# Kernel optimization log

Hardware: AMD Instinct MI355X
Metric: run time of the kernel (lower is better)

Reference implementation:

```python
import jax, jax.numpy as jnp
import numpy as np

DEPTH, HEADS, K, EPS = 4, 8, 3, 1e-5
DIM, CIN, COUT = 128, 64, 64


def conv1x1(x, w, b=None):
    y = jnp.einsum('oi,bihw->bohw', w, x)
    return y if b is None else y + b[None, :, None, None]


def dilated_conv3x3(x, w, b, d):
    y = jax.lax.conv_general_dilated(
        x, w, window_strides=(1, 1), padding=[(d, d), (d, d)],
        rhs_dilation=(d, d), dimension_numbers=('NCHW', 'OIHW', 'NCHW'))
    return y + b[None, :, None, None]


def batchnorm_train(x, g, b):
    # BatchNorm2d in training mode: biased batch stats over (B,H,W)
    mu = jnp.mean(x, axis=(0, 2, 3), keepdims=True)
    var = jnp.var(x, axis=(0, 2, 3), keepdims=True)
    return (x - mu) * jax.lax.rsqrt(var + EPS) * g[None, :, None, None] + b[None, :, None, None]


def unfold3(x):
    # nn.Unfold(k=3, pad=1): (B,C,H,W) -> (B,C,k*k,H,W), patch index row-major (dy,dx)
    B, C, H, W = x.shape
    p = K // 2
    xp = jnp.pad(x, ((0, 0), (0, 0), (p, p), (p, p)))
    return jnp.stack([xp[:, :, dy:dy + H, dx:dx + W]
                      for dy in range(K) for dx in range(K)], axis=2)


def local_self_attention(x, qkv_w, fc_w, fc_b):
    B, C, H, W = x.shape
    c = C // HEADS
    scale = c ** -0.5
    qkv = conv1x1(x, qkv_w)                      # (B,3C,H,W)
    q, k, v = jnp.split(qkv, 3, axis=1)
    shape6 = lambda t: unfold3(t).reshape(B, HEADS, c, K * K, H, W)
    q, k, v = shape6(q) * scale, shape6(k), shape6(v)
    # NOTE: original einsum labels dim2 (channels/head) as n/m and dim3 (k^2) as the
    # contracted axis, i.e. channel-attention contracted over the 9 patch positions.
    dots = jnp.einsum('bhnkij,bhmkij->bhnmij', q, k)   # (B,h,c,c,H,W)
    attn = jax.nn.softmax(dots, axis=3)
    out = jnp.einsum('bhnmij,bhmkij->bhnkij', attn, v)  # (B,h,c,k^2,H,W)
    out = out.reshape(B, C, K * K, H, W).sum(axis=2)
    return conv1x1(out, fc_w, fc_b) + x


def setup_inputs() -> dict:
    key = jax.random.key(0)
    ks = jax.random.split(key, 12)
    s = 0.05
    return {
        'x': jax.random.normal(ks[0], (2, CIN, 96, 96), jnp.float32),
        'w_in': jax.random.normal(ks[1], (DIM, CIN), jnp.float32) * s,
        'b_in': jnp.zeros((DIM,), jnp.float32),
        'conv_w': jax.random.normal(ks[2], (DEPTH, DIM, DIM, 3, 3), jnp.float32) * s,
        'conv_b': jnp.zeros((DEPTH, DIM), jnp.float32),
        'bn_g': jnp.ones((DEPTH, DIM), jnp.float32),
        'bn_b': jnp.zeros((DEPTH, DIM), jnp.float32),
        'qkv_w': jax.random.normal(ks[3], (DEPTH, 3 * DIM, DIM), jnp.float32) * s,
        'fc_w': jax.random.normal(ks[4], (DEPTH, DIM, DIM), jnp.float32) * s,
        'fc_b': jnp.zeros((DEPTH, DIM), jnp.float32),
        'w_out': jax.random.normal(ks[5], (COUT, DIM), jnp.float32) * s,
        'b_out': jnp.zeros((COUT,), jnp.float32),
    }


def reference(x, w_in, b_in, conv_w, conv_b, bn_g, bn_b, qkv_w, fc_w, fc_b, w_out, b_out):
    h = conv1x1(x, w_in, b_in)
    for i in range(DEPTH):
        d = 2 ** i
        h = jax.nn.relu(batchnorm_train(dilated_conv3x3(h, conv_w[i], conv_b[i], d), bn_g[i], bn_b[i]))
        h = local_self_attention(h, qkv_w[i], fc_w[i], fc_b[i])
    return conv1x1(h, w_out, b_out)
```

## Files before the change

kernel.cpp:

```cpp
#include <hip/hip_runtime.h>
#include <math.h>

typedef __attribute__((ext_vector_type(8))) short bf16x8;
typedef __attribute__((ext_vector_type(4))) float f32x4;
typedef __attribute__((ext_vector_type(4))) unsigned short us4;
typedef __attribute__((ext_vector_type(8))) unsigned short us8;

constexpr int BB = 2;
constexpr int CC = 128;
constexpr int HH = 96, WW = 96;
constexpr int PP = HH * WW;
constexpr int NN = BB * PP;
constexpr int CONV_BLKS = NN / 48;

__device__ __forceinline__ float bf2f(unsigned short u) {
    return __uint_as_float(((unsigned)u) << 16);
}
__device__ __forceinline__ unsigned short f2bf(float f) {
    unsigned u = __float_as_uint(f);
    unsigned r = u + 0x7fff + ((u >> 16) & 1);
    return (unsigned short)(r >> 16);
}

__global__ __launch_bounds__(256)
void k_wconv(const float* __restrict__ conv_w, const float* __restrict__ qkv_w,
             const float* __restrict__ fc_w, const float* __restrict__ w_in,
             const float* __restrict__ w_out,
             unsigned short* __restrict__ wcv, unsigned short* __restrict__ wqkv,
             unsigned short* __restrict__ wfc, unsigned short* __restrict__ wi,
             unsigned short* __restrict__ wo)
{
    int gid = blockIdx.x * 256 + threadIdx.x;
    if (gid < 589824) {
        int L = gid / 147456, r = gid % 147456;
        int o = r / 1152, k = r % 1152;
        int t = k / 128, c = k % 128;
        float v = conv_w[(((size_t)(L * 128 + o) * 128 + c) * 9) + t];
        wcv[gid] = f2bf(v);
    } else if (gid < 786432) {
        int g = gid - 589824;
        int o = (g % 49152) / 128;
        float v = qkv_w[g] * (o < 128 ? 0.25f : 1.0f);
        wqkv[g] = f2bf(v);
    } else if (gid < 851968) {
        int g = gid - 786432;
        wfc[g] = f2bf(fc_w[g]);
    } else if (gid < 860160) {
        int g = gid - 851968;
        wi[g] = f2bf(w_in[g]);
    } else if (gid < 868352) {
        int g = gid - 860160;
        wo[g] = f2bf(w_out[g]);
    }
}

__global__ __launch_bounds__(256)
void k_xconv(const float* __restrict__ x, unsigned short* __restrict__ xT)
{
    int n = blockIdx.x * 256 + threadIdx.x;
    int b = n / PP, p = n - b * PP;
    unsigned short* dst = xT + (size_t)n * 64;
    #pragma unroll
    for (int cg = 0; cg < 16; ++cg) {
        us4 st;
        #pragma unroll
        for (int r = 0; r < 4; ++r)
            st[r] = f2bf(x[((size_t)(b * 64 + cg * 4 + r)) * PP + p]);
        *reinterpret_cast<us4*>(dst + cg * 4) = st;
    }
}

template<int DIL>
__global__ __launch_bounds__(384)
void k_conv(const unsigned short* __restrict__ W,
            const unsigned short* __restrict__ act,
            float* __restrict__ y,
            float* __restrict__ parts,
            const unsigned short* __restrict__ zp)
{
    int tid = threadIdx.x;
    int lane = tid & 63, wv = tid >> 6;
    int wm = wv & 1, wz = wv >> 1;
    int l15 = lane & 15, kg = lane >> 4;

    int n_base = blockIdx.x * 48;
    int o_base = wm * 64;

    const unsigned short* wbase[4];
    #pragma unroll
    for (int fm = 0; fm < 4; ++fm)
        wbase[fm] = W + (size_t)(o_base + fm * 16 + l15) * 1152 + kg * 8;

    const unsigned short* bbase[3];
    int iF[3], jF[3];
    #pragma unroll
    for (int fn = 0; fn < 3; ++fn) {
        int n = n_base + fn * 16 + l15;
        bbase[fn] = act + (size_t)n * 128 + kg * 8;
        int pix = n % PP;
        iF[fn] = pix / WW;
        jF[fn] = pix % WW;
    }

    f32x4 acc[4][3];
    #pragma unroll
    for (int fm = 0; fm < 4; ++fm)
        #pragma unroll
        for (int fn = 0; fn < 3; ++fn)
            acc[fm][fn] = (f32x4){0.f, 0.f, 0.f, 0.f};

    const unsigned short* zpk = zp + kg * 8;
    int t0 = wz * 3;
    #pragma unroll
    for (int tt = 0; tt < 3; ++tt) {
        int t = t0 + tt;
        int oy = (t / 3 - 1) * DIL, ox = (t % 3 - 1) * DIL;
        int disp = (oy * WW + ox) * 128;
        const unsigned short* baddr[3];
        #pragma unroll
        for (int fn = 0; fn < 3; ++fn) {
            bool v = ((unsigned)(iF[fn] + oy) < (unsigned)HH) &&
                     ((unsigned)(jF[fn] + ox) < (unsigned)WW);
            baddr[fn] = v ? (bbase[fn] + disp) : zpk;
        }
        #pragma unroll
        for (int c0 = 0; c0 < 128; c0 += 32) {
            bf16x8 a[4], b[3];
            #pragma unroll
            for (int fm = 0; fm < 4; ++fm)
                a[fm] = *reinterpret_cast<const bf16x8*>(wbase[fm] + t * 128 + c0);
            #pragma unroll
            for (int fn = 0; fn < 3; ++fn)
                b[fn] = *reinterpret_cast<const bf16x8*>(baddr[fn] + c0);
            #pragma unroll
            for (int fm = 0; fm < 4; ++fm)
                #pragma unroll
                for (int fn = 0; fn < 3; ++fn)
                    acc[fm][fn] = __builtin_amdgcn_mfma_f32_16x16x32_bf16(
                        a[fm], b[fn], acc[fm][fn], 0, 0, 0);
        }
    }

    __shared__ float red[4][48][64];
    if (wz) {
        int s = wm * 2 + wz - 1;
        #pragma unroll
        for (int fm = 0; fm < 4; ++fm)
            #pragma unroll
            for (int fn = 0; fn < 3; ++fn)
                #pragma unroll
                for (int r = 0; r < 4; ++r)
                    red[s][fm * 12 + fn * 4 + r][lane] = acc[fm][fn][r];
    }
    __syncthreads();
    if (wz == 0) {
        #pragma unroll
        for (int fm = 0; fm < 4; ++fm)
            #pragma unroll
            for (int fn = 0; fn < 3; ++fn)
                #pragma unroll
                for (int r = 0; r < 4; ++r)
                    acc[fm][fn][r] += red[wm * 2][fm * 12 + fn * 4 + r][lane] +
                                      red[wm * 2 + 1][fm * 12 + fn * 4 + r][lane];

        #pragma unroll
        for (int fm = 0; fm < 4; ++fm) {
            int o0 = o_base + fm * 16 + kg * 4;
            #pragma unroll
            for (int fn = 0; fn < 3; ++fn) {
                int n = n_base + fn * 16 + l15;
                *reinterpret_cast<f32x4*>(y + (size_t)n * 128 + o0) = acc[fm][fn];
            }
        }

        #pragma unroll
        for (int fm = 0; fm < 4; ++fm) {
            #pragma unroll
            for (int r = 0; r < 4; ++r) {
                float s = 0.f, s2 = 0.f;
                #pragma unroll
                for (int fn = 0; fn < 3; ++fn) {
                    float v = acc[fm][fn][r];
                    s += v; s2 += v * v;
                }
                #pragma unroll
                for (int m = 1; m <= 8; m <<= 1) {
                    s  += __shfl_xor(s,  m, 64);
                    s2 += __shfl_xor(s2, m, 64);
                }
                if (l15 == 0) {
                    int c = o_base + fm * 16 + kg * 4 + r;
                    parts[(size_t)blockIdx.x * 256 + c]       = s;
                    parts[(size_t)blockIdx.x * 256 + 128 + c] = s2;
                }
            }
        }
    }
}

template<int WM, int WN, int F, int MODE>
__global__ __launch_bounds__(WM * WN * 64)
void k_gemm(const unsigned short* __restrict__ W,
            const unsigned short* __restrict__ act,
            const float* __restrict__ bias,
            const unsigned short* __restrict__ resid,
            void* __restrict__ outp,
            int Kw, int Cin, int Cout)
{
    int tid = threadIdx.x;
    int lane = tid & 63, wv = tid >> 6;
    int wm = wv % WM, wn = wv / WM;
    int l15 = lane & 15, kg = lane >> 4;

    int n_base = blockIdx.x * (WN * 16 * F) + wn * 16 * F;
    int o_base = blockIdx.y * (WM * 64) + wm * 64;

    const unsigned short* wbase[4];
    #pragma unroll
    for (int fm = 0; fm < 4; ++fm) {
        int o = o_base + fm * 16 + l15;
        wbase[fm] = W + (size_t)o * Kw + kg * 8;
    }

    const unsigned short* bbase[F];
    #pragma unroll
    for (int fn = 0; fn < F; ++fn) {
        int n = n_base + fn * 16 + l15;
        bbase[fn] = act + (size_t)n * Cin + kg * 8;
    }

    f32x4 acc[4][F];
    #pragma unroll
    for (int fm = 0; fm < 4; ++fm)
        #pragma unroll
        for (int fn = 0; fn < F; ++fn)
            acc[fm][fn] = (f32x4){0.f, 0.f, 0.f, 0.f};

    #pragma unroll
    for (int k0 = 0; k0 < 128; k0 += 32) {
        if (k0 >= Cin) break;
        bf16x8 a[4], b[F];
        #pragma unroll
        for (int fm = 0; fm < 4; ++fm)
            a[fm] = *reinterpret_cast<const bf16x8*>(wbase[fm] + k0);
        #pragma unroll
        for (int fn = 0; fn < F; ++fn)
            b[fn] = *reinterpret_cast<const bf16x8*>(bbase[fn] + k0);
        #pragma unroll
        for (int fm = 0; fm < 4; ++fm)
            #pragma unroll
            for (int fn = 0; fn < F; ++fn)
                acc[fm][fn] = __builtin_amdgcn_mfma_f32_16x16x32_bf16(
                    a[fm], b[fn], acc[fm][fn], 0, 0, 0);
    }

    #pragma unroll
    for (int fm = 0; fm < 4; ++fm) {
        #pragma unroll
        for (int fn = 0; fn < F; ++fn) {
            f32x4 v = acc[fm][fn];
            int n = n_base + fn * 16 + l15;
            int o0 = o_base + fm * 16 + kg * 4;
            if constexpr (MODE == 0 || MODE == 2) {
                if (bias) {
                    #pragma unroll
                    for (int r = 0; r < 4; ++r) v[r] += bias[o0 + r];
                }
                if constexpr (MODE == 2) {
                    us4 rv = *reinterpret_cast<const us4*>(resid + (size_t)n * Cout + o0);
                    #pragma unroll
                    for (int r = 0; r < 4; ++r) v[r] += bf2f(rv[r]);
                }
                us4 st;
                #pragma unroll
                for (int r = 0; r < 4; ++r) st[r] = f2bf(v[r]);
                *reinterpret_cast<us4*>((unsigned short*)outp + (size_t)n * Cout + o0) = st;
            } else {
                int b_ = n / PP, p = n - b_ * PP;
                float* op = (float*)outp;
                #pragma unroll
                for (int r = 0; r < 4; ++r)
                    op[((size_t)(b_ * Cout + o0 + r)) * PP + p] = v[r] + bias[o0 + r];
            }
        }
    }
}

__global__ __launch_bounds__(384)
void k_bnfin(const float* __restrict__ partials, const float* __restrict__ g,
             const float* __restrict__ b, float* __restrict__ scsh)
{
    int c = blockIdx.x;
    int t = threadIdx.x;
    float s  = partials[(size_t)t * 256 + c];
    float s2 = partials[(size_t)t * 256 + 128 + c];
    #pragma unroll
    for (int m = 32; m > 0; m >>= 1) {
        s  += __shfl_down(s,  m, 64);
        s2 += __shfl_down(s2, m, 64);
    }
    __shared__ float ls[6], ls2[6];
    int wid = t >> 6;
    if ((t & 63) == 0) { ls[wid] = s; ls2[wid] = s2; }
    __syncthreads();
    if (t == 0) {
        float S = 0.f, S2 = 0.f;
        #pragma unroll
        for (int w = 0; w < 6; ++w) { S += ls[w]; S2 += ls2[w]; }
        const float inv = 1.f / (float)NN;
        float mu = S * inv;
        float var = S2 * inv - mu * mu;
        float sc = g[c] * rsqrtf(var + 1e-5f);
        scsh[c] = sc;
        scsh[128 + c] = b[c] - mu * sc;
    }
}

__global__ __launch_bounds__(256)
void k_bnrelu(const float* __restrict__ y, const float* __restrict__ scsh,
              unsigned short* __restrict__ h)
{
    int gid = blockIdx.x * 256 + threadIdx.x;
    int c0 = (gid * 4) & 127;
    size_t idx = (size_t)gid * 4;
    f32x4 v = *reinterpret_cast<const f32x4*>(y + idx);
    us4 st;
    #pragma unroll
    for (int r = 0; r < 4; ++r) {
        float f = fmaxf(fmaf(v[r], scsh[c0 + r], scsh[128 + c0 + r]), 0.f);
        st[r] = f2bf(f);
    }
    *reinterpret_cast<us4*>(h + idx) = st;
}

__global__ __launch_bounds__(256)
void k_attn(const unsigned short* __restrict__ qkv, unsigned short* __restrict__ att)
{
    int gid = blockIdx.x * 256 + threadIdx.x;
    int ng   = gid & 3;
    int head = (gid >> 2) & 7;
    int n    = gid >> 5;
    int pix = n % PP;
    int i = pix / WW, j = pix % WW;
    int hc = head * 16;
    const unsigned short* base = qkv + (size_t)n * 384;

    float dots[4][16];
    float vs[16];
    #pragma unroll
    for (int m = 0; m < 16; ++m) vs[m] = 0.f;
    #pragma unroll
    for (int nn = 0; nn < 4; ++nn)
        #pragma unroll
        for (int m = 0; m < 16; ++m) dots[nn][m] = 0.f;

    #pragma unroll
    for (int dy = 0; dy < 3; ++dy) {
        #pragma unroll
        for (int dx = 0; dx < 3; ++dx) {
            if (!(((unsigned)(i + dy - 1) < (unsigned)HH) &&
                  ((unsigned)(j + dx - 1) < (unsigned)WW))) continue;
            const unsigned short* pb = base + ((dy - 1) * WW + (dx - 1)) * 384;
            us4 q4 = *reinterpret_cast<const us4*>(pb + hc + ng * 4);
            us8 k0 = *reinterpret_cast<const us8*>(pb + 128 + hc);
            us8 k1 = *reinterpret_cast<const us8*>(pb + 128 + hc + 8);
            us8 v0 = *reinterpret_cast<const us8*>(pb + 256 + hc);
            us8 v1 = *reinterpret_cast<const us8*>(pb + 256 + hc + 8);
            float kf[16];
            #pragma unroll
            for (int e = 0; e < 8; ++e) {
                kf[e] = bf2f(k0[e]);
                kf[8 + e] = bf2f(k1[e]);
                vs[e] += bf2f(v0[e]);
                vs[8 + e] += bf2f(v1[e]);
            }
            #pragma unroll
            for (int nn = 0; nn < 4; ++nn) {
                float qf = bf2f(q4[nn]);
                #pragma unroll
                for (int m = 0; m < 16; ++m)
                    dots[nn][m] = fmaf(qf, kf[m], dots[nn][m]);
            }
        }
    }

    us4 st;
    #pragma unroll
    for (int nn = 0; nn < 4; ++nn) {
        float mx = dots[nn][0];
        #pragma unroll
        for (int m = 1; m < 16; ++m) mx = fmaxf(mx, dots[nn][m]);
        float den = 0.f, o = 0.f;
        #pragma unroll
        for (int m = 0; m < 16; ++m) {
            float e = __expf(dots[nn][m] - mx);
            den += e;
            o = fmaf(e, vs[m], o);
        }
        st[nn] = f2bf(o / den);
    }
    *reinterpret_cast<us4*>(att + (size_t)n * CC + hc + ng * 4) = st;
}

extern "C" void kernel_launch(void* const* d_in, const int* in_sizes, int n_in,
                              void* d_out, int out_size, void* d_ws, size_t ws_size,
                              hipStream_t stream)
{
    const float* x      = (const float*)d_in[0];
    const float* w_in   = (const float*)d_in[1];
    const float* b_in   = (const float*)d_in[2];
    const float* conv_w = (const float*)d_in[3];
    const float* bn_g   = (const float*)d_in[5];
    const float* bn_b   = (const float*)d_in[6];
    const float* qkv_w  = (const float*)d_in[7];
    const float* fc_w   = (const float*)d_in[8];
    const float* fc_b   = (const float*)d_in[9];
    const float* w_out  = (const float*)d_in[10];
    const float* b_out  = (const float*)d_in[11];

    char* ws = (char*)d_ws;
    unsigned short* zp    = (unsigned short*)(ws);
    unsigned short* wcv   = (unsigned short*)(ws + 4096);
    unsigned short* wqkv  = (unsigned short*)(ws + 1183744);
    unsigned short* wfc   = (unsigned short*)(ws + 1576960);
    unsigned short* wi    = (unsigned short*)(ws + 1708032);
    unsigned short* wo    = (unsigned short*)(ws + 1724416);
    unsigned short* xT    = (unsigned short*)(ws + 1740800);
    unsigned short* bufA  = (unsigned short*)(ws + 4100096);
    float*          ybuf  = (float*)        (ws + 8818688);
    unsigned short* hbuf  = (unsigned short*)(ws + 18255872);
    unsigned short* qkvb  = (unsigned short*)(ws + 22974464);
    unsigned short* attb  = (unsigned short*)(ws + 37130240);
    float*          parts = (float*)        (ws + 41848832);
    float*          scsh  = (float*)        (ws + 42242048);

    hipMemsetAsync(zp, 0, 4096, stream);

    k_wconv<<<3392, 256, 0, stream>>>(conv_w, qkv_w, fc_w, w_in, w_out,
                                      wcv, wqkv, wfc, wi, wo);
    k_xconv<<<NN / 256, 256, 0, stream>>>(x, xT);

    k_gemm<1, 2, 3, 0><<<dim3(192, 2), 128, 0, stream>>>(
        wi, xT, b_in, nullptr, bufA, 64, 64, 128);

    for (int L = 0; L < 4; ++L) {
        const unsigned short* wc = wcv + (size_t)L * 147456;
        switch (L) {
            case 0: k_conv<1><<<CONV_BLKS, 384, 0, stream>>>(wc, bufA, ybuf, parts, zp); break;
            case 1: k_conv<2><<<CONV_BLKS, 384, 0, stream>>>(wc, bufA, ybuf, parts, zp); break;
            case 2: k_conv<4><<<CONV_BLKS, 384, 0, stream>>>(wc, bufA, ybuf, parts, zp); break;
            case 3: k_conv<8><<<CONV_BLKS, 384, 0, stream>>>(wc, bufA, ybuf, parts, zp); break;
        }
        k_bnfin<<<128, 384, 0, stream>>>(parts, bn_g + L * 128, bn_b + L * 128, scsh);
        k_bnrelu<<<2304, 256, 0, stream>>>(ybuf, scsh, hbuf);

        k_gemm<1, 2, 3, 0><<<dim3(192, 6), 128, 0, stream>>>(
            wqkv + (size_t)L * 49152, hbuf, nullptr, nullptr, qkvb, 128, 128, 384);

        k_attn<<<2304, 256, 0, stream>>>(qkvb, attb);

        k_gemm<1, 2, 3, 2><<<dim3(192, 2), 128, 0, stream>>>(
            wfc + (size_t)L * 16384, attb, fc_b + L * 128, hbuf, bufA, 128, 128, 128);
    }

    k_gemm<1, 2, 3, 3><<<dim3(192, 1), 128, 0, stream>>>(
        wo, bufA, b_out, nullptr, (float*)d_out, 128, 128, 64);
}
```

Before: 465.4 us.

## Fuse local attention with fc projection and split conv output channels across grid

The attention kernel now writes its per-pixel outputs into a swizzled shared-memory tile and immediately runs the 128x128 fc projection with MFMA, adding bias and residual before storing. This removes the attention intermediate buffer round trip and one kernel launch per layer. Separately, the dilated conv kernel now splits the two 64-channel output halves across a second grid dimension with 192-thread blocks instead of one 384-thread block. That doubles the block count and halves shared memory per block, at the cost of reading each activation tile twice.

Result: no change. 474.4 us (+1.9%).

```diff
diff --git a/kernel.cpp b/kernel.cpp
--- a/kernel.cpp
+++ b/kernel.cpp
@@ -71,7 +71,7 @@
 }
 
 template<int DIL>
-__global__ __launch_bounds__(384)
+__global__ __launch_bounds__(192)
 void k_conv(const unsigned short* __restrict__ W,
             const unsigned short* __restrict__ act,
             float* __restrict__ y,
@@ -79,12 +79,11 @@
             const unsigned short* __restrict__ zp)
 {
     int tid = threadIdx.x;
-    int lane = tid & 63, wv = tid >> 6;
-    int wm = wv & 1, wz = wv >> 1;
+    int lane = tid & 63, wz = tid >> 6;
     int l15 = lane & 15, kg = lane >> 4;
 
     int n_base = blockIdx.x * 48;
-    int o_base = wm * 64;
+    int o_base = blockIdx.y * 64;
 
     const unsigned short* wbase[4];
     #pragma unroll
@@ -141,16 +140,15 @@
         }
     }
 
-    __shared__ float red[4][48][64];
+    __shared__ float red[2][48][64];
     if (wz) {
-        int s = wm * 2 + wz - 1;
         #pragma unroll
         for (int fm = 0; fm < 4; ++fm)
             #pragma unroll
             for (int fn = 0; fn < 3; ++fn)
                 #pragma unroll
                 for (int r = 0; r < 4; ++r)
-                    red[s][fm * 12 + fn * 4 + r][lane] = acc[fm][fn][r];
+                    red[wz - 1][fm * 12 + fn * 4 + r][lane] = acc[fm][fn][r];
     }
     __syncthreads();
     if (wz == 0) {
@@ -160,8 +158,8 @@
             for (int fn = 0; fn < 3; ++fn)
                 #pragma unroll
                 for (int r = 0; r < 4; ++r)
-                    acc[fm][fn][r] += red[wm * 2][fm * 12 + fn * 4 + r][lane] +
-                                      red[wm * 2 + 1][fm * 12 + fn * 4 + r][lane];
+                    acc[fm][fn][r] += red[0][fm * 12 + fn * 4 + r][lane] +
+                                      red[1][fm * 12 + fn * 4 + r][lane];
 
         #pragma unroll
         for (int fm = 0; fm < 4; ++fm) {
@@ -203,7 +201,6 @@
 void k_gemm(const unsigned short* __restrict__ W,
             const unsigned short* __restrict__ act,
             const float* __restrict__ bias,
-            const unsigned short* __restrict__ resid,
             void* __restrict__ outp,
             int Kw, int Cin, int Cout)
 {
@@ -261,15 +258,10 @@
             f32x4 v = acc[fm][fn];
             int n = n_base + fn * 16 + l15;
             int o0 = o_base + fm * 16 + kg * 4;
-            if constexpr (MODE == 0 || MODE == 2) {
+            if constexpr (MODE == 0) {
                 if (bias) {
                     #pragma unroll
                     for (int r = 0; r < 4; ++r) v[r] += bias[o0 + r];
-                }
-                if constexpr (MODE == 2) {
-                    us4 rv = *reinterpret_cast<const us4*>(resid + (size_t)n * Cout + o0);
-                    #pragma unroll
-                    for (int r = 0; r < 4; ++r) v[r] += bf2f(rv[r]);
                 }
                 us4 st;
                 #pragma unroll
@@ -334,72 +326,139 @@
 }
 
 __global__ __launch_bounds__(256)
-void k_attn(const unsigned short* __restrict__ qkv, unsigned short* __restrict__ att)
-{
-    int gid = blockIdx.x * 256 + threadIdx.x;
-    int ng   = gid & 3;
-    int head = (gid >> 2) & 7;
-    int n    = gid >> 5;
-    int pix = n % PP;
-    int i = pix / WW, j = pix % WW;
-    int hc = head * 16;
-    const unsigned short* base = qkv + (size_t)n * 384;
-
-    float dots[4][16];
-    float vs[16];
-    #pragma unroll
-    for (int m = 0; m < 16; ++m) vs[m] = 0.f;
-    #pragma unroll
-    for (int nn = 0; nn < 4; ++nn)
-        #pragma unroll
-        for (int m = 0; m < 16; ++m) dots[nn][m] = 0.f;
-
-    #pragma unroll
-    for (int dy = 0; dy < 3; ++dy) {
-        #pragma unroll
-        for (int dx = 0; dx < 3; ++dx) {
-            if (!(((unsigned)(i + dy - 1) < (unsigned)HH) &&
-                  ((unsigned)(j + dx - 1) < (unsigned)WW))) continue;
-            const unsigned short* pb = base + ((dy - 1) * WW + (dx - 1)) * 384;
-            us4 q4 = *reinterpret_cast<const us4*>(pb + hc + ng * 4);
-            us8 k0 = *reinterpret_cast<const us8*>(pb + 128 + hc);
-            us8 k1 = *reinterpret_cast<const us8*>(pb + 128 + hc + 8);
-            us8 v0 = *reinterpret_cast<const us8*>(pb + 256 + hc);
-            us8 v1 = *reinterpret_cast<const us8*>(pb + 256 + hc + 8);
-            float kf[16];
-            #pragma unroll
-            for (int e = 0; e < 8; ++e) {
-                kf[e] = bf2f(k0[e]);
-                kf[8 + e] = bf2f(k1[e]);
-                vs[e] += bf2f(v0[e]);
-                vs[8 + e] += bf2f(v1[e]);
+void k_attnfc(const unsigned short* __restrict__ qkv,
+              const unsigned short* __restrict__ wfc,
+              const float* __restrict__ fcb,
+              const unsigned short* __restrict__ resid,
+              unsigned short* __restrict__ out)
+{
+    __shared__ unsigned short atile[32 * 128];
+    int tid = threadIdx.x;
+    int n_base = blockIdx.x * 32;
+
+    #pragma unroll 1
+    for (int u = 0; u < 4; ++u) {
+        int unit = u * 256 + tid;
+        int pl   = unit >> 5;
+        int head = (unit >> 2) & 7;
+        int ng   = unit & 3;
+        int n    = n_base + pl;
+        int pix  = n % PP;
+        int i = pix / WW, j = pix % WW;
+        int hc = head * 16;
+        const unsigned short* base = qkv + (size_t)n * 384;
+
+        float dots[4][16];
+        float vs[16];
+        #pragma unroll
+        for (int m = 0; m < 16; ++m) vs[m] = 0.f;
+        #pragma unroll
+        for (int nn = 0; nn < 4; ++nn)
+            #pragma unroll
+            for (int m = 0; m < 16; ++m) dots[nn][m] = 0.f;
+
+        #pragma unroll
+        for (int dy = 0; dy < 3; ++dy) {
+            #pragma unroll
+            for (int dx = 0; dx < 3; ++dx) {
+                if (!(((unsigned)(i + dy - 1) < (unsigned)HH) &&
+                      ((unsigned)(j + dx - 1) < (unsigned)WW))) continue;
+                const unsigned short* pb = base + ((dy - 1) * WW + (dx - 1)) * 384;
+                us4 q4 = *reinterpret_cast<const us4*>(pb + hc + ng * 4);
+                us8 k0 = *reinterpret_cast<const us8*>(pb + 128 + hc);
+                us8 k1 = *reinterpret_cast<const us8*>(pb + 128 + hc + 8);
+                us8 v0 = *reinterpret_cast<const us8*>(pb + 256 + hc);
+                us8 v1 = *reinterpret_cast<const us8*>(pb + 256 + hc + 8);
+                float kf[16];
+                #pragma unroll
+                for (int e = 0; e < 8; ++e) {
+                    kf[e] = bf2f(k0[e]);
+                    kf[8 + e] = bf2f(k1[e]);
+                    vs[e] += bf2f(v0[e]);
+                    vs[8 + e] += bf2f(v1[e]);
+                }
+                #pragma unroll
+                for (int nn = 0; nn < 4; ++nn) {
+                    float qf = bf2f(q4[nn]);
+                    #pragma unroll
+                    for (int m = 0; m < 16; ++m)
+                        dots[nn][m] = fmaf(qf, kf[m], dots[nn][m]);
+                }
             }
-            #pragma unroll
-            for (int nn = 0; nn < 4; ++nn) {
-                float qf = bf2f(q4[nn]);
-                #pragma unroll
-                for (int m = 0; m < 16; ++m)
-                    dots[nn][m] = fmaf(qf, kf[m], dots[nn][m]);
+        }
+
+        us4 st;
+        #pragma unroll
+        for (int nn = 0; nn < 4; ++nn) {
+            float mx = dots[nn][0];
+            #pragma unroll
+            for (int m = 1; m < 16; ++m) mx = fmaxf(mx, dots[nn][m]);
+            float den = 0.f, o = 0.f;
+            #pragma unroll
+            for (int m = 0; m < 16; ++m) {
+                float e = __expf(dots[nn][m] - mx);
+                den += e;
+                o = fmaf(e, vs[m], o);
             }
-        }
-    }
-
-    us4 st;
-    #pragma unroll
-    for (int nn = 0; nn < 4; ++nn) {
-        float mx = dots[nn][0];
-        #pragma unroll
-        for (int m = 1; m < 16; ++m) mx = fmaxf(mx, dots[nn][m]);
-        float den = 0.f, o = 0.f;
-        #pragma unroll
-        for (int m = 0; m < 16; ++m) {
-            float e = __expf(dots[nn][m] - mx);
-            den += e;
-            o = fmaf(e, vs[m], o);
-        }
-        st[nn] = f2bf(o / den);
-    }
-    *reinterpret_cast<us4*>(att + (size_t)n * CC + hc + ng * 4) = st;
+            st[nn] = f2bf(o / den);
+        }
+        int off = (pl * 256 + (hc + ng * 4) * 2) ^ ((pl & 7) << 4);
+        *reinterpret_cast<us4*>(reinterpret_cast<char*>(atile) + off) = st;
+    }
+    __syncthreads();
+
+    int lane = tid & 63, wvv = tid >> 6;
+    int l15 = lane & 15, kg = lane >> 4;
+    int o_base = wvv * 32;
+
+    const unsigned short* wbase[2];
+    #pragma unroll
+    for (int fm = 0; fm < 2; ++fm)
+        wbase[fm] = wfc + (size_t)(o_base + fm * 16 + l15) * 128 + kg * 8;
+
+    f32x4 acc[2][2];
+    #pragma unroll
+    for (int fm = 0; fm < 2; ++fm)
+        #pragma unroll
+        for (int fn = 0; fn < 2; ++fn)
+            acc[fm][fn] = (f32x4){0.f, 0.f, 0.f, 0.f};
+
+    #pragma unroll
+    for (int k0 = 0; k0 < 128; k0 += 32) {
+        bf16x8 a[2], b[2];
+        #pragma unroll
+        for (int fm = 0; fm < 2; ++fm)
+            a[fm] = *reinterpret_cast<const bf16x8*>(wbase[fm] + k0);
+        #pragma unroll
+        for (int fn = 0; fn < 2; ++fn) {
+            int pl2 = fn * 16 + l15;
+            int off = (pl2 * 256 + (k0 + kg * 8) * 2) ^ ((pl2 & 7) << 4);
+            b[fn] = *reinterpret_cast<const bf16x8*>(reinterpret_cast<char*>(atile) + off);
+        }
+        #pragma unroll
+        for (int fm = 0; fm < 2; ++fm)
+            #pragma unroll
+            for (int fn = 0; fn < 2; ++fn)
+                acc[fm][fn] = __builtin_amdgcn_mfma_f32_16x16x32_bf16(
+                    a[fm], b[fn], acc[fm][fn], 0, 0, 0);
+    }
+
+    #pragma unroll
+    for (int fm = 0; fm < 2; ++fm) {
+        #pragma unroll
+        for (int fn = 0; fn < 2; ++fn) {
+            f32x4 v = acc[fm][fn];
+            int n = n_base + fn * 16 + l15;
+            int o0 = o_base + fm * 16 + kg * 4;
+            us4 rv = *reinterpret_cast<const us4*>(resid + (size_t)n * 128 + o0);
+            #pragma unroll
+            for (int r = 0; r < 4; ++r) v[r] += fcb[o0 + r] + bf2f(rv[r]);
+            us4 st;
+            #pragma unroll
+            for (int r = 0; r < 4; ++r) st[r] = f2bf(v[r]);
+            *reinterpret_cast<us4*>(out + (size_t)n * 128 + o0) = st;
+        }
+    }
 }
 
 extern "C" void kernel_launch(void* const* d_in, const int* in_sizes, int n_in,
@@ -430,7 +489,6 @@
     float*          ybuf  = (float*)        (ws + 8818688);
     unsigned short* hbuf  = (unsigned short*)(ws + 18255872);
     unsigned short* qkvb  = (unsigned short*)(ws + 22974464);
-    unsigned short* attb  = (unsigned short*)(ws + 37130240);
     float*          parts = (float*)        (ws + 41848832);
     float*          scsh  = (float*)        (ws + 42242048);
 
@@ -441,28 +499,26 @@
     k_xconv<<<NN / 256, 256, 0, stream>>>(x, xT);
 
     k_gemm<1, 2, 3, 0><<<dim3(192, 2), 128, 0, stream>>>(
-        wi, xT, b_in, nullptr, bufA, 64, 64, 128);
+        wi, xT, b_in, bufA, 64, 64, 128);
 
     for (int L = 0; L < 4; ++L) {
         const unsigned short* wc = wcv + (size_t)L * 147456;
         switch (L) {
-            case 0: k_conv<1><<<CONV_BLKS, 384, 0, stream>>>(wc, bufA, ybuf, parts, zp); break;
-            case 1: k_conv<2><<<CONV_BLKS, 384, 0, stream>>>(wc, bufA, ybuf, parts, zp); break;
-            case 2: k_conv<4><<<CONV_BLKS, 384, 0, stream>>>(wc, bufA, ybuf, parts, zp); break;
-            case 3: k_conv<8><<<CONV_BLKS, 384, 0, stream>>>(wc, bufA, ybuf, parts, zp); break;
+            case 0: k_conv<1><<<dim3(CONV_BLKS, 2), 192, 0, stream>>>(wc, bufA, ybuf, parts, zp); break;
+            case 1: k_conv<2><<<dim3(CONV_BLKS, 2), 192, 0, stream>>>(wc, bufA, ybuf, parts, zp); break;
+            case 2: k_conv<4><<<dim3(CONV_BLKS, 2), 192, 0, stream>>>(wc, bufA, ybuf, parts, zp); break;
+            case 3: k_conv<8><<<dim3(CONV_BLKS, 2), 192, 0, stream>>>(wc, bufA, ybuf, parts, zp); break;
         }
         k_bnfin<<<128, 384, 0, stream>>>(parts, bn_g + L * 128, bn_b + L * 128, scsh);
         k_bnrelu<<<2304, 256, 0, stream>>>(ybuf, scsh, hbuf);
 
         k_gemm<1, 2, 3, 0><<<dim3(192, 6), 128, 0, stream>>>(
-            wqkv + (size_t)L * 49152, hbuf, nullptr, nullptr, qkvb, 128, 128, 384);
-
-        k_attn<<<2304, 256, 0, stream>>>(qkvb, attb);
-
-        k_gemm<1, 2, 3, 2><<<dim3(192, 2), 128, 0, stream>>>(
-            wfc + (size_t)L * 16384, attb, fc_b + L * 128, hbuf, bufA, 128, 128, 128);
+            wqkv + (size_t)L * 49152, hbuf, nullptr, qkvb, 128, 128, 384);
+
+        k_attnfc<<<576, 256, 0, stream>>>(
+            qkvb, wfc + (size_t)L * 16384, fc_b + L * 128, hbuf, bufA);
     }
 
     k_gemm<1, 2, 3, 3><<<dim3(192, 1), 128, 0, stream>>>(
-        wo, bufA, b_out, nullptr, (float*)d_out, 128, 128, 64);
-}
+        wo, bufA, b_out, (float*)d_out, 128, 128, 64);
+}
```

## Stage attention rows in LDS and split conv blocks over output channels

Applied to the files above, without the earlier changes.

The local attention kernel now has each block load a three-row band of q/k/v for one head pair into shared memory. Its 3x3 neighbourhood reads then come from LDS rather than repeatedly from global memory. The dilated conv kernel moves the two output-channel halves from separate waves in one 384-thread block to a second grid dimension of 192-thread blocks, which halves the reduction scratch and doubles the block count. The roughly 60 KB LDS tile per attention block limits how many blocks fit on a CU, and each conv block now reloads its activation tile for each output half.

After: 462.2 us. About the same (-0.7%).

```diff
diff --git a/kernel.cpp b/kernel.cpp
--- a/kernel.cpp
+++ b/kernel.cpp
@@ -71,7 +71,7 @@
 }
 
 template<int DIL>
-__global__ __launch_bounds__(384)
+__global__ __launch_bounds__(192)
 void k_conv(const unsigned short* __restrict__ W,
             const unsigned short* __restrict__ act,
             float* __restrict__ y,
@@ -79,12 +79,11 @@
             const unsigned short* __restrict__ zp)
 {
     int tid = threadIdx.x;
-    int lane = tid & 63, wv = tid >> 6;
-    int wm = wv & 1, wz = wv >> 1;
+    int lane = tid & 63, wz = tid >> 6;
     int l15 = lane & 15, kg = lane >> 4;
 
     int n_base = blockIdx.x * 48;
-    int o_base = wm * 64;
+    int o_base = blockIdx.y * 64;
 
     const unsigned short* wbase[4];
     #pragma unroll
@@ -141,16 +140,15 @@
         }
     }
 
-    __shared__ float red[4][48][64];
+    __shared__ float red[2][48][64];
     if (wz) {
-        int s = wm * 2 + wz - 1;
         #pragma unroll
         for (int fm = 0; fm < 4; ++fm)
             #pragma unroll
             for (int fn = 0; fn < 3; ++fn)
                 #pragma unroll
                 for (int r = 0; r < 4; ++r)
-                    red[s][fm * 12 + fn * 4 + r][lane] = acc[fm][fn][r];
+                    red[wz - 1][fm * 12 + fn * 4 + r][lane] = acc[fm][fn][r];
     }
     __syncthreads();
     if (wz == 0) {
@@ -160,8 +158,8 @@
             for (int fn = 0; fn < 3; ++fn)
                 #pragma unroll
                 for (int r = 0; r < 4; ++r)
-                    acc[fm][fn][r] += red[wm * 2][fm * 12 + fn * 4 + r][lane] +
-                                      red[wm * 2 + 1][fm * 12 + fn * 4 + r][lane];
+                    acc[fm][fn][r] += red[0][fm * 12 + fn * 4 + r][lane] +
+                                      red[1][fm * 12 + fn * 4 + r][lane];
 
         #pragma unroll
         for (int fm = 0; fm < 4; ++fm) {
@@ -334,72 +332,98 @@
 }
 
 __global__ __launch_bounds__(256)
-void k_attn(const unsigned short* __restrict__ qkv, unsigned short* __restrict__ att)
-{
-    int gid = blockIdx.x * 256 + threadIdx.x;
-    int ng   = gid & 3;
-    int head = (gid >> 2) & 7;
-    int n    = gid >> 5;
-    int pix = n % PP;
-    int i = pix / WW, j = pix % WW;
-    int hc = head * 16;
-    const unsigned short* base = qkv + (size_t)n * 384;
-
-    float dots[4][16];
-    float vs[16];
-    #pragma unroll
-    for (int m = 0; m < 16; ++m) vs[m] = 0.f;
-    #pragma unroll
-    for (int nn = 0; nn < 4; ++nn)
-        #pragma unroll
-        for (int m = 0; m < 16; ++m) dots[nn][m] = 0.f;
-
-    #pragma unroll
-    for (int dy = 0; dy < 3; ++dy) {
-        #pragma unroll
-        for (int dx = 0; dx < 3; ++dx) {
-            if (!(((unsigned)(i + dy - 1) < (unsigned)HH) &&
-                  ((unsigned)(j + dx - 1) < (unsigned)WW))) continue;
-            const unsigned short* pb = base + ((dy - 1) * WW + (dx - 1)) * 384;
-            us4 q4 = *reinterpret_cast<const us4*>(pb + hc + ng * 4);
-            us8 k0 = *reinterpret_cast<const us8*>(pb + 128 + hc);
-            us8 k1 = *reinterpret_cast<const us8*>(pb + 128 + hc + 8);
-            us8 v0 = *reinterpret_cast<const us8*>(pb + 256 + hc);
-            us8 v1 = *reinterpret_cast<const us8*>(pb + 256 + hc + 8);
-            float kf[16];
-            #pragma unroll
-            for (int e = 0; e < 8; ++e) {
-                kf[e] = bf2f(k0[e]);
-                kf[8 + e] = bf2f(k1[e]);
-                vs[e] += bf2f(v0[e]);
-                vs[8 + e] += bf2f(v1[e]);
-            }
-            #pragma unroll
-            for (int nn = 0; nn < 4; ++nn) {
-                float qf = bf2f(q4[nn]);
-                #pragma unroll
-                for (int m = 0; m < 16; ++m)
-                    dots[nn][m] = fmaf(qf, kf[m], dots[nn][m]);
-            }
-        }
-    }
-
-    us4 st;
-    #pragma unroll
-    for (int nn = 0; nn < 4; ++nn) {
-        float mx = dots[nn][0];
-        #pragma unroll
-        for (int m = 1; m < 16; ++m) mx = fmaxf(mx, dots[nn][m]);
-        float den = 0.f, o = 0.f;
-        #pragma unroll
-        for (int m = 0; m < 16; ++m) {
-            float e = __expf(dots[nn][m] - mx);
-            den += e;
-            o = fmaf(e, vs[m], o);
-        }
-        st[nn] = f2bf(o / den);
-    }
-    *reinterpret_cast<us4*>(att + (size_t)n * CC + hc + ng * 4) = st;
+void k_attn2(const unsigned short* __restrict__ qkv, unsigned short* __restrict__ att)
+{
+    __shared__ unsigned short tile[288 * 104];
+    int tid = threadIdx.x;
+    int br = blockIdx.x;
+    int hp = blockIdx.y;
+    int b = br / HH, i = br - (br / HH) * HH;
+
+    #pragma unroll 1
+    for (int it = 0; it < 14; ++it) {
+        int idx = it * 256 + tid;
+        if (idx < 3456) {
+            int pp = idx / 12;
+            int rem = idx - pp * 12;
+            int s = rem >> 2, u8 = rem & 3;
+            int rr = pp / 96, col = pp - rr * 96;
+            int ai = i + rr - 1;
+            us8 val = {0, 0, 0, 0, 0, 0, 0, 0};
+            if ((unsigned)ai < (unsigned)HH) {
+                int n = b * PP + ai * WW + col;
+                val = *reinterpret_cast<const us8*>(
+                    qkv + (size_t)n * 384 + s * 128 + hp * 32 + u8 * 8);
+            }
+            *reinterpret_cast<us8*>(tile + pp * 104 + s * 32 + u8 * 8) = val;
+        }
+    }
+    __syncthreads();
+
+    #pragma unroll 1
+    for (int u = 0; u < 3; ++u) {
+        int unit = u * 256 + tid;
+        int j  = unit >> 3;
+        int h  = (unit >> 2) & 1;
+        int ng = unit & 3;
+
+        float dots[4][16];
+        float vs[16];
+        #pragma unroll
+        for (int m = 0; m < 16; ++m) vs[m] = 0.f;
+        #pragma unroll
+        for (int nn = 0; nn < 4; ++nn)
+            #pragma unroll
+            for (int m = 0; m < 16; ++m) dots[nn][m] = 0.f;
+
+        #pragma unroll 1
+        for (int rr = 0; rr < 3; ++rr) {
+            #pragma unroll
+            for (int dj = -1; dj <= 1; ++dj) {
+                int jj = j + dj;
+                if ((unsigned)jj >= (unsigned)WW) continue;
+                const unsigned short* pb = tile + (rr * 96 + jj) * 104 + h * 16;
+                us4 q4 = *reinterpret_cast<const us4*>(pb + ng * 4);
+                us8 k0 = *reinterpret_cast<const us8*>(pb + 32);
+                us8 k1 = *reinterpret_cast<const us8*>(pb + 40);
+                us8 v0 = *reinterpret_cast<const us8*>(pb + 64);
+                us8 v1 = *reinterpret_cast<const us8*>(pb + 72);
+                float kf[16];
+                #pragma unroll
+                for (int e = 0; e < 8; ++e) {
+                    kf[e] = bf2f(k0[e]);
+                    kf[8 + e] = bf2f(k1[e]);
+                    vs[e] += bf2f(v0[e]);
+                    vs[8 + e] += bf2f(v1[e]);
+                }
+                #pragma unroll
+                for (int nn = 0; nn < 4; ++nn) {
+                    float qf = bf2f(q4[nn]);
+                    #pragma unroll
+                    for (int m = 0; m < 16; ++m)
+                        dots[nn][m] = fmaf(qf, kf[m], dots[nn][m]);
+                }
+            }
+        }
+
+        us4 st;
+        #pragma unroll
+        for (int nn = 0; nn < 4; ++nn) {
+            float mx = dots[nn][0];
+            #pragma unroll
+            for (int m = 1; m < 16; ++m) mx = fmaxf(mx, dots[nn][m]);
+            float den = 0.f, o = 0.f;
+            #pragma unroll
+            for (int m = 0; m < 16; ++m) {
+                float e = __expf(dots[nn][m] - mx);
+                den += e;
+                o = fmaf(e, vs[m], o);
+            }
+            st[nn] = f2bf(o / den);
+        }
+        int n = b * PP + i * WW + j;
+        *reinterpret_cast<us4*>(att + (size_t)n * CC + hp * 32 + h * 16 + ng * 4) = st;
+    }
 }
 
 extern "C" void kernel_launch(void* const* d_in, const int* in_sizes, int n_in,
@@ -446,10 +470,10 @@
     for (int L = 0; L < 4; ++L) {
         const unsigned short* wc = wcv + (size_t)L * 147456;
         switch (L) {
-            case 0: k_conv<1><<<CONV_BLKS, 384, 0, stream>>>(wc, bufA, ybuf, parts, zp); break;
-            case 1: k_conv<2><<<CONV_BLKS, 384, 0, stream>>>(wc, bufA, ybuf, parts, zp); break;
-            case 2: k_conv<4><<<CONV_BLKS, 384, 0, stream>>>(wc, bufA, ybuf, parts, zp); break;
-            case 3: k_conv<8><<<CONV_BLKS, 384, 0, stream>>>(wc, bufA, ybuf, parts, zp); break;
+            case 0: k_conv<1><<<dim3(CONV_BLKS, 2), 192, 0, stream>>>(wc, bufA, ybuf, parts, zp); break;
+            case 1: k_conv<2><<<dim3(CONV_BLKS, 2), 192, 0, stream>>>(wc, bufA, ybuf, parts, zp); break;
+            case 2: k_conv<4><<<dim3(CONV_BLKS, 2), 192, 0, stream>>>(wc, bufA, ybuf, parts, zp); break;
+            case 3: k_conv<8><<<dim3(CONV_BLKS, 2), 192, 0, stream>>>(wc, bufA, ybuf, parts, zp); break;
         }
         k_bnfin<<<128, 384, 0, stream>>>(parts, bn_g + L * 128, bn_b + L * 128, scsh);
         k_bnrelu<<<2304, 256, 0, stream>>>(ybuf, scsh, hbuf);
@@ -457,7 +481,7 @@
         k_gemm<1, 2, 3, 0><<<dim3(192, 6), 128, 0, stream>>>(
             wqkv + (size_t)L * 49152, hbuf, nullptr, nullptr, qkvb, 128, 128, 384);
 
-        k_attn<<<2304, 256, 0, stream>>>(qkvb, attb);
+        k_attn2<<<dim3(BB * HH, 4), 256, 0, stream>>>(qkvb, attb);
 
         k_gemm<1, 2, 3, 2><<<dim3(192, 2), 128, 0, stream>>>(
             wfc + (size_t)L * 16384, attb, fc_b + L * 128, hbuf, bufA, 128, 128, 128);
```
